# Kernel tuning notes

Hardware: AMD Instinct MI355X
Metric: run time of the kernel (lower is better)

The kernel has to match this reference:

```python
import jax, jax.numpy as jnp
import numpy as np

N_NODES = 5000
N_EDGES = 80000
HIDDEN = 128
NUM_RBF = 64
MAX_Z = 128
CUTOFF_UPPER = 5.0
LN_EPS = 1e-5


def setup_inputs() -> dict:
    key = jax.random.key(0)
    ks = jax.random.split(key, 24)
    H, R = HIDDEN, NUM_RBF
    def lin(k, out_d, in_d):
        s = 1.0 / np.sqrt(in_d)
        return jax.random.uniform(k, (out_d, in_d), jnp.float32, -s, s)
    def bias(k, out_d, in_d):
        s = 1.0 / np.sqrt(in_d)
        return jax.random.uniform(k, (out_d,), jnp.float32, -s, s)
    v = jax.random.normal(ks[3], (N_EDGES, 3), jnp.float32)
    v = v / jnp.linalg.norm(v, axis=-1, keepdims=True)
    return {
        "z": jax.random.randint(ks[0], (N_NODES,), 0, MAX_Z),
        "edge_index": jax.random.randint(ks[1], (2, N_EDGES), 0, N_NODES),
        "edge_weight": jax.random.uniform(ks[2], (N_EDGES,), jnp.float32) * CUTOFF_UPPER * 0.9,
        "edge_vec_norm": v,
        "edge_attr": jax.random.normal(ks[4], (N_EDGES, R), jnp.float32),
        "emb": jax.random.normal(ks[5], (MAX_Z, H), jnp.float32),
        "W_emb2": lin(ks[6], H, 2 * H), "b_emb2": bias(ks[7], H, 2 * H),
        "Wd1": lin(ks[8], H, R), "bd1": bias(ks[9], H, R),
        "Wd2": lin(ks[10], H, R), "bd2": bias(ks[11], H, R),
        "Wd3": lin(ks[12], H, R), "bd3": bias(ks[13], H, R),
        "Wt1": lin(ks[14], H, H), "Wt2": lin(ks[15], H, H), "Wt3": lin(ks[16], H, H),
        "Ws1": lin(ks[17], 2 * H, H), "bs1": bias(ks[18], 2 * H, H),
        "Ws2": lin(ks[19], 3 * H, 2 * H), "bs2": bias(ks[20], 3 * H, 2 * H),
        "ln_g": jnp.ones((H,), jnp.float32),
        "ln_b": jnp.zeros((H,), jnp.float32),
    }


def _skew(v):
    # v: [E,3] -> [E,3,3] skew-symmetric
    z = jnp.zeros_like(v[:, 0])
    return jnp.stack(
        [z, -v[:, 2], v[:, 1], v[:, 2], z, -v[:, 0], -v[:, 1], v[:, 0], z], axis=1
    ).reshape(-1, 3, 3)


def _sym(v):
    # symmetric traceless part of outer product (outer product already symmetric)
    outer = v[:, :, None] * v[:, None, :]
    tr = jnp.trace(outer, axis1=-2, axis2=-1) / 3.0
    return outer - tr[:, None, None] * jnp.eye(3, dtype=v.dtype)


def reference(z, edge_index, edge_weight, edge_vec_norm, edge_attr,
              emb, W_emb2, b_emb2, Wd1, bd1, Wd2, bd2, Wd3, bd3,
              Wt1, Wt2, Wt3, Ws1, bs1, Ws2, bs2, ln_g, ln_b):
    N = z.shape[0]
    H = emb.shape[1]
    src, dst = edge_index[0], edge_index[1]

    # atomic number message Zij: [E,H]
    Z = emb[z]
    Zij = jnp.concatenate([Z[src], Z[dst]], axis=-1) @ W_emb2.T + b_emb2

    # cosine cutoff (cutoff_lower = 0)
    cut = 0.5 * (jnp.cos(edge_weight * (jnp.pi / CUTOFF_UPPER)) + 1.0)
    cut = cut * (edge_weight < CUTOFF_UPPER).astype(edge_weight.dtype)
    C = cut[:, None] * Zij  # [E,H]

    f1 = (edge_attr @ Wd1.T + bd1) * C  # [E,H]
    f2 = (edge_attr @ Wd2.T + bd2) * C
    f3 = (edge_attr @ Wd3.T + bd3) * C

    eye = jnp.eye(3, dtype=C.dtype)
    Iij = f1[:, :, None, None] * eye  # [E,H,3,3]
    Aij = f2[:, :, None, None] * _skew(edge_vec_norm)[:, None, :, :]
    Sij = f3[:, :, None, None] * _sym(edge_vec_norm)[:, None, :, :]

    I = jax.ops.segment_sum(Iij, src, num_segments=N)  # [N,H,3,3]
    A = jax.ops.segment_sum(Aij, src, num_segments=N)
    S = jax.ops.segment_sum(Sij, src, num_segments=N)

    # Frobenius norm per channel, LayerNorm, scalar MLP
    tn = ((I + A + S) ** 2).sum((-2, -1))  # [N,H]
    mu = tn.mean(-1, keepdims=True)
    var = tn.var(-1, keepdims=True)
    norm = (tn - mu) / jnp.sqrt(var + LN_EPS) * ln_g + ln_b
    norm = jax.nn.silu(norm @ Ws1.T + bs1)
    norm = jax.nn.silu(norm @ Ws2.T + bs2)
    norm = norm.reshape(N, H, 3)

    I = jnp.einsum('nhij,gh->ngij', I, Wt1) * norm[:, :, 0, None, None]
    A = jnp.einsum('nhij,gh->ngij', A, Wt2) * norm[:, :, 1, None, None]
    S = jnp.einsum('nhij,gh->ngij', S, Wt3) * norm[:, :, 2, None, None]
    return I + A + S
```

## Files before the change

kernel.cpp:

```cpp
#include <hip/hip_runtime.h>
#include <hip/hip_bf16.h>

#define NN   5000
#define NP   5008
#define NE   80000
#define HID  128
#define NRBF 64
#define PI_OVER_5 0.6283185307179586f
#define LN_EPS 1e-5f

typedef unsigned short bf16_t;
typedef __attribute__((ext_vector_type(8))) short short8;
typedef __attribute__((ext_vector_type(4))) float floatx4;

__device__ __forceinline__ bf16_t to_bf16(float x){
    union { float f; unsigned int u; } v; v.f = x;
    unsigned int r = v.u + 0x7fffu + ((v.u >> 16) & 1u);
    return (bf16_t)(r >> 16);
}
__device__ __forceinline__ float from_bf16(bf16_t h){
    union { unsigned int u; float f; } v; v.u = ((unsigned int)h) << 16;
    return v.f;
}
__device__ __forceinline__ uint4 pack8(const float* s){
    float4 a = *(const float4*)s;
    float4 b = *(const float4*)(s + 4);
    uint4 o;
    o.x = to_bf16(a.x) | ((unsigned)to_bf16(a.y) << 16);
    o.y = to_bf16(a.z) | ((unsigned)to_bf16(a.w) << 16);
    o.z = to_bf16(b.x) | ((unsigned)to_bf16(b.y) << 16);
    o.w = to_bf16(b.z) | ((unsigned)to_bf16(b.w) << 16);
    return o;
}
__device__ __forceinline__ short8 cvt8(float4 a, float4 b){
    short8 r;
    r[0] = (short)to_bf16(a.x); r[1] = (short)to_bf16(a.y);
    r[2] = (short)to_bf16(a.z); r[3] = (short)to_bf16(a.w);
    r[4] = (short)to_bf16(b.x); r[5] = (short)to_bf16(b.y);
    r[6] = (short)to_bf16(b.z); r[7] = (short)to_bf16(b.w);
    return r;
}

__global__ __launch_bounds__(256) void k_prep(
    const float* __restrict__ Wd1, const float* __restrict__ Wd2, const float* __restrict__ Wd3,
    const float* __restrict__ bd1, const float* __restrict__ bd2, const float* __restrict__ bd3,
    const float* __restrict__ Wt1, const float* __restrict__ Wt2, const float* __restrict__ Wt3,
    const float* __restrict__ Ws1, const float* __restrict__ Ws2,
    const float* __restrict__ W_emb2, const float* __restrict__ emb,
    bf16_t* __restrict__ Wcat, bf16_t* __restrict__ Wtc,
    bf16_t* __restrict__ Ws1b, bf16_t* __restrict__ Ws2b, float* __restrict__ bdcat,
    float* __restrict__ embL, float* __restrict__ embR)
{
    int b = blockIdx.x, tid = threadIdx.x;
    if (b < 100){
        int t = b * 256 + tid;
        int i8 = t * 8;
        const float* src; bf16_t* dst;
        if (i8 < 24576){
            int j = i8; int tb = j >> 13; int r = j & 8191;
            src = ((tb == 0) ? Wd1 : (tb == 1) ? Wd2 : Wd3) + r; dst = Wcat + j;
        } else if (i8 < 24576 + 49152){
            int j = i8 - 24576; int tb = j >> 14; int r = j & 16383;
            src = ((tb == 0) ? Wt1 : (tb == 1) ? Wt2 : Wt3) + r; dst = Wtc + j;
        } else if (i8 < 24576 + 49152 + 32768){
            int j = i8 - 73728; src = Ws1 + j; dst = Ws1b + j;
        } else {
            int j = i8 - 106496; src = Ws2 + j; dst = Ws2b + j;
        }
        *(uint4*)dst = pack8(src);
        if (t < 384){
            int tb2 = t >> 7, ch2 = t & 127;
            const float* bsrc = (tb2 == 0) ? bd1 : ((tb2 == 1) ? bd2 : bd3);
            bdcat[t] = bsrc[ch2];
        }
    } else {
        int t = b - 100;
        int half = tid >> 7;
        int h = tid & 127;
        const float* wl = W_emb2 + (size_t)h * (2 * HID) + half * HID;
        const float* er = emb + t * HID;
        float s = 0.f;
        #pragma unroll 8
        for (int k = 0; k < HID; k++) s += wl[k] * er[k];
        (half ? embR : embL)[t * HID + h] = s;
    }
}

__global__ void k_count(const int* __restrict__ ei, int* __restrict__ counts){
    int e = blockIdx.x * 256 + threadIdx.x;
    if (e < NE) atomicAdd(&counts[ei[e]], 1);
}

__global__ __launch_bounds__(1024) void k_scan(
    const int* __restrict__ counts, int* __restrict__ offsets, int* __restrict__ cursor)
{
    __shared__ int s[1024];
    const int t = threadIdx.x;
    const int CH = 5;
    int base = t * CH;
    int loc[CH];
    int lsum = 0;
    #pragma unroll
    for (int u = 0; u < CH; u++){
        int i = base + u;
        int v = (i < NN) ? counts[i] : 0;
        loc[u] = lsum;
        lsum += v;
    }
    s[t] = lsum;
    __syncthreads();
    for (int d = 1; d < 1024; d <<= 1){
        int v = (t >= d) ? s[t - d] : 0;
        __syncthreads();
        s[t] += v;
        __syncthreads();
    }
    int excl = s[t] - lsum;
    #pragma unroll
    for (int u = 0; u < CH; u++){
        int i = base + u;
        if (i < NN){ int o = excl + loc[u]; offsets[i] = o; cursor[i] = o; }
    }
    if (t == 1023) offsets[NN] = s[1023];
}

__global__ void k_fill(const int* __restrict__ ei, const int* __restrict__ z,
                       const float* __restrict__ ew, const float* __restrict__ evn,
                       int* __restrict__ cursor, int* __restrict__ elist,
                       float2* __restrict__ meta, float* __restrict__ evn_p){
    int e = blockIdx.x * 256 + threadIdx.x;
    if (e < NE){
        int sN = ei[e], dN = ei[NE + e];
        int p = atomicAdd(&cursor[sN], 1);
        elist[p] = e;
        float w = ew[e];
        float c = (w < 5.0f) ? 0.5f * (__cosf(w * PI_OVER_5) + 1.0f) : 0.0f;
        meta[p] = make_float2(c, __int_as_float(z[sN] | (z[dN] << 8)));
        evn_p[p*3+0] = evn[e*3+0];
        evn_p[p*3+1] = evn[e*3+1];
        evn_p[p*3+2] = evn[e*3+2];
    }
}

__global__ __launch_bounds__(256) void k_edge_gather(
    const int* __restrict__ offs, const int* __restrict__ elist,
    const float2* __restrict__ meta, const float* __restrict__ evn_p,
    const float* __restrict__ attr,
    const bf16_t* __restrict__ Wcat, const float* __restrict__ bdcat,
    const float* __restrict__ embL, const float* __restrict__ embR,
    const float* __restrict__ b_emb2,
    const float* __restrict__ ln_g, const float* __restrict__ ln_b,
    bf16_t* __restrict__ accb, bf16_t* __restrict__ lnb)
{
    __shared__ __align__(16) float4 sV[64];
    __shared__ int   sZZ[64];
    __shared__ float sAcc[10][132];
    __shared__ float sRed[8];

    const int tid = threadIdx.x;
    const int wv = tid >> 6, lane = tid & 63;
    const int col = lane & 15, q = lane >> 4;
    const int n = blockIdx.x;
    const int s = offs[n], e_end = offs[n + 1];

    short8 bfr[6][2];
    float bdv[3][2], bev[2];
    #pragma unroll
    for (int cg = 0; cg < 2; cg++){
        int ch = wv * 32 + cg * 16 + col;
        bev[cg] = b_emb2[ch];
        #pragma unroll
        for (int t = 0; t < 3; t++){
            bdv[t][cg] = bdcat[t * 128 + ch];
            #pragma unroll
            for (int s2 = 0; s2 < 2; s2++)
                bfr[t * 2 + cg][s2] = *(const short8*)(Wcat + (size_t)(t * 128 + ch) * NRBF + s2 * 32 + q * 8);
        }
    }

    float pl[10][2];
    #pragma unroll
    for (int p = 0; p < 10; p++){ pl[p][0] = 0.f; pl[p][1] = 0.f; }

    for (int c0 = s; c0 < e_end; c0 += 64){
        __syncthreads();
        if (tid < 64){
            int pos = c0 + tid;
            if (pos < e_end){
                float2 m = meta[pos];
                sV[tid]  = make_float4(evn_p[pos*3+0], evn_p[pos*3+1], evn_p[pos*3+2], m.x);
                sZZ[tid] = __float_as_int(m.y);
            } else {
                sV[tid]  = make_float4(0.f, 0.f, 0.f, 0.f);
                sZZ[tid] = 0;
            }
        }
        __syncthreads();
        int nch = e_end - c0; if (nch > 64) nch = 64;
        int ntiles = (nch + 15) >> 4;
        for (int t16 = 0; t16 < ntiles; t16++){
            int pos = c0 + t16 * 16 + col;
            int cpos = (pos < e_end) ? pos : (e_end - 1);
            int e = elist[cpos];
            const float* ar = attr + (size_t)e * NRBF + q * 8;
            short8 af[2];
            #pragma unroll
            for (int s2 = 0; s2 < 2; s2++){
                float4 u0 = *(const float4*)(ar + s2 * 32);
                float4 u1 = *(const float4*)(ar + s2 * 32 + 4);
                af[s2] = cvt8(u0, u1);
            }
            floatx4 D[3][2];
            #pragma unroll
            for (int t = 0; t < 3; t++)
                #pragma unroll
                for (int cg = 0; cg < 2; cg++){
                    floatx4 d = (floatx4)(0.f);
                    d = __builtin_amdgcn_mfma_f32_16x16x32_bf16(af[0], bfr[t*2+cg][0], d, 0, 0, 0);
                    d = __builtin_amdgcn_mfma_f32_16x16x32_bf16(af[1], bfr[t*2+cg][1], d, 0, 0, 0);
                    D[t][cg] = d;
                }
            #pragma unroll
            for (int r = 0; r < 4; r++){
                int eslot = t16 * 16 + q * 4 + r;
                float4 vv = sV[eslot];
                int zp = sZZ[eslot];
                int zs = zp & 255, zd = zp >> 8;
                float vx = vv.x, vy = vv.y, vz = vv.z, cut = vv.w;
                float xx = vx*vx, yy = vy*vy, zz = vz*vz;
                float t3 = (xx + yy + zz) * (1.f/3.f);
                float gxx = xx - t3, gyy = yy - t3, gzz = zz - t3;
                float gxy = vx*vy, gxz = vx*vz, gyz = vy*vz;
                #pragma unroll
                for (int cg = 0; cg < 2; cg++){
                    int ch = wv * 32 + cg * 16 + col;
                    float L = embL[zs * HID + ch];
                    float R = embR[zd * HID + ch];
                    float Cv = cut * (L + R + bev[cg]);
                    float f1 = (D[0][cg][r] + bdv[0][cg]) * Cv;
                    float f2 = (D[1][cg][r] + bdv[1][cg]) * Cv;
                    float f3 = (D[2][cg][r] + bdv[2][cg]) * Cv;
                    pl[0][cg] += f1;
                    pl[1][cg] += f2 * vx; pl[2][cg] += f2 * vy; pl[3][cg] += f2 * vz;
                    pl[4][cg] += f3 * gxx; pl[5][cg] += f3 * gyy; pl[6][cg] += f3 * gzz;
                    pl[7][cg] += f3 * gxy; pl[8][cg] += f3 * gxz; pl[9][cg] += f3 * gyz;
                }
            }
        }
    }

    #pragma unroll
    for (int p = 0; p < 10; p++)
        #pragma unroll
        for (int cg = 0; cg < 2; cg++){
            float v = pl[p][cg];
            v += __shfl_xor(v, 16);
            v += __shfl_xor(v, 32);
            pl[p][cg] = v;
        }
    if (lane < 16){
        #pragma unroll
        for (int p = 0; p < 10; p++){
            sAcc[p][wv * 32 + 0  + lane] = pl[p][0];
            sAcc[p][wv * 32 + 16 + lane] = pl[p][1];
        }
    }
    __syncthreads();

    float av[10]; float tn = 0.f;
    const int ch = tid;
    if (tid < 128){
        #pragma unroll
        for (int p = 0; p < 10; p++) av[p] = sAcc[p][ch];
        tn = 3.f*av[0]*av[0] + 2.f*av[0]*(av[4]+av[5]+av[6])
           + av[4]*av[4] + av[5]*av[5] + av[6]*av[6]
           + 2.f*(av[7]*av[7] + av[8]*av[8] + av[9]*av[9])
           + 2.f*(av[1]*av[1] + av[2]*av[2] + av[3]*av[3]);
    }
    float s1 = tn, s2 = tn * tn;
    #pragma unroll
    for (int d = 1; d < 64; d <<= 1){
        s1 += __shfl_xor(s1, d);
        s2 += __shfl_xor(s2, d);
    }
    if (lane == 0){ sRed[wv] = s1; sRed[4 + wv] = s2; }
    __syncthreads();
    if (tid < 128){
        float mu  = (sRed[0] + sRed[1]) * (1.f / HID);
        float var = (sRed[4] + sRed[5]) * (1.f / HID) - mu * mu;
        float ln = (tn - mu) * rsqrtf(var + LN_EPS) * ln_g[ch] + ln_b[ch];
        lnb[(size_t)n * HID + ch] = to_bf16(ln);
        #pragma unroll
        for (int p = 0; p < 10; p++)
            accb[(size_t)p * NP * HID + (size_t)n * HID + ch] = to_bf16(av[p]);
    }
}

__global__ __launch_bounds__(256) void k_node(
    const bf16_t* __restrict__ lnb, const bf16_t* __restrict__ accb,
    const bf16_t* __restrict__ Ws1b, const float* __restrict__ bs1,
    const bf16_t* __restrict__ Ws2b, const float* __restrict__ bs2,
    const bf16_t* __restrict__ Wtc,
    float* __restrict__ out)
{
    __shared__ __align__(16) bf16_t h1s[16 * 280];
    __shared__ float nrms[16 * 392];

    const int tid = threadIdx.x;
    const int wv = tid >> 6, lane = tid & 63;
    const int col = lane & 15, q = lane >> 4;
    const int n0 = blockIdx.x * 16;

    {
        short8 a1[4];
        #pragma unroll
        for (int k = 0; k < 4; k++)
            a1[k] = *(const short8*)(lnb + (size_t)(n0 + col) * HID + k * 32 + q * 8);
        floatx4 c1[4];
        #pragma unroll
        for (int nt = 0; nt < 4; nt++) c1[nt] = (floatx4)(0.f);
        #pragma unroll
        for (int nt = 0; nt < 4; nt++){
            int cg = wv * 64 + nt * 16 + col;
            #pragma unroll
            for (int k = 0; k < 4; k++){
                short8 b = *(const short8*)(Ws1b + (size_t)cg * HID + k * 32 + q * 8);
                c1[nt] = __builtin_amdgcn_mfma_f32_16x16x32_bf16(a1[k], b, c1[nt], 0, 0, 0);
            }
        }
        #pragma unroll
        for (int nt = 0; nt < 4; nt++){
            int cg = wv * 64 + nt * 16 + col;
            float bias = bs1[cg];
            #pragma unroll
            for (int r = 0; r < 4; r++){
                float v = c1[nt][r] + bias;
                v = v / (1.f + __expf(-v));
                h1s[(q * 4 + r) * 280 + cg] = to_bf16(v);
            }
        }
    }
    __syncthreads();

    {
        short8 a2[8];
        #pragma unroll
        for (int k = 0; k < 8; k++)
            a2[k] = *(const short8*)&h1s[col * 280 + k * 32 + q * 8];
        floatx4 c2[6];
        #pragma unroll
        for (int nt = 0; nt < 6; nt++) c2[nt] = (floatx4)(0.f);
        #pragma unroll
        for (int nt = 0; nt < 6; nt++){
            int cg = wv * 96 + nt * 16 + col;
            #pragma unroll
            for (int k = 0; k < 8; k++){
                short8 b = *(const short8*)(Ws2b + (size_t)cg * 256 + k * 32 + q * 8);
                c2[nt] = __builtin_amdgcn_mfma_f32_16x16x32_bf16(a2[k], b, c2[nt], 0, 0, 0);
            }
        }
        #pragma unroll
        for (int nt = 0; nt < 6; nt++){
            int cg = wv * 96 + nt * 16 + col;
            float bias = bs2[cg];
            #pragma unroll
            for (int r = 0; r < 4; r++){
                float v = c2[nt][r] + bias;
                v = v / (1.f + __expf(-v));
                nrms[(q * 4 + r) * 392 + cg] = v;
            }
        }
    }
    __syncthreads();

    floatx4 cm[10][2];
    #pragma unroll
    for (int p = 0; p < 10; p++){
        #pragma unroll
        for (int nt = 0; nt < 2; nt++) cm[p][nt] = (floatx4)(0.f);
    }
    #pragma unroll
    for (int p = 0; p < 10; p++){
        const bf16_t* ap = accb + (size_t)p * NP * HID + (size_t)(n0 + col) * HID;
        short8 a3[4];
        #pragma unroll
        for (int k = 0; k < 4; k++)
            a3[k] = *(const short8*)(ap + k * 32 + q * 8);
        int tb = (p == 0) ? 0 : ((p < 4) ? 1 : 2);
        #pragma unroll
        for (int nt = 0; nt < 2; nt++){
            int g = wv * 32 + nt * 16 + col;
            const bf16_t* wp = Wtc + tb * 16384 + (size_t)g * HID;
            #pragma unroll
            for (int k = 0; k < 4; k++){
                short8 b = *(const short8*)(wp + k * 32 + q * 8);
                cm[p][nt] = __builtin_amdgcn_mfma_f32_16x16x32_bf16(a3[k], b, cm[p][nt], 0, 0, 0);
            }
        }
    }
    #pragma unroll
    for (int nt = 0; nt < 2; nt++){
        int g = wv * 32 + nt * 16 + col;
        #pragma unroll
        for (int r = 0; r < 4; r++){
            int node = q * 4 + r;
            int n = n0 + node;
            if (n < NN){
                float n0f = nrms[node * 392 + g * 3 + 0];
                float n1f = nrms[node * 392 + g * 3 + 1];
                float n2f = nrms[node * 392 + g * 3 + 2];
                float c   = cm[0][nt][r];
                float ax  = cm[1][nt][r], ay = cm[2][nt][r], az = cm[3][nt][r];
                float sxx = cm[4][nt][r], syy= cm[5][nt][r], szz= cm[6][nt][r];
                float sxy = cm[7][nt][r], sxz= cm[8][nt][r], syz= cm[9][nt][r];
                float* o = out + ((size_t)n * HID + g) * 9;
                o[0] = n0f*c + n2f*sxx;   o[1] = n2f*sxy - n1f*az;  o[2] = n2f*sxz + n1f*ay;
                o[3] = n2f*sxy + n1f*az;  o[4] = n0f*c + n2f*syy;   o[5] = n2f*syz - n1f*ax;
                o[6] = n2f*sxz - n1f*ay;  o[7] = n2f*syz + n1f*ax;  o[8] = n0f*c + n2f*szz;
            }
        }
    }
}

extern "C" void kernel_launch(void* const* d_in, const int* in_sizes, int n_in,
                              void* d_out, int out_size, void* d_ws, size_t ws_size,
                              hipStream_t stream)
{
    (void)in_sizes; (void)n_in; (void)out_size; (void)ws_size;
    const int*   z      = (const int*)  d_in[0];
    const int*   ei     = (const int*)  d_in[1];
    const float* ew     = (const float*)d_in[2];
    const float* evn    = (const float*)d_in[3];
    const float* attr   = (const float*)d_in[4];
    const float* emb    = (const float*)d_in[5];
    const float* W_emb2 = (const float*)d_in[6];
    const float* b_emb2 = (const float*)d_in[7];
    const float* Wd1 = (const float*)d_in[8];  const float* bd1 = (const float*)d_in[9];
    const float* Wd2 = (const float*)d_in[10]; const float* bd2 = (const float*)d_in[11];
    const float* Wd3 = (const float*)d_in[12]; const float* bd3 = (const float*)d_in[13];
    const float* Wt1 = (const float*)d_in[14]; const float* Wt2 = (const float*)d_in[15];
    const float* Wt3 = (const float*)d_in[16];
    const float* Ws1 = (const float*)d_in[17]; const float* bs1 = (const float*)d_in[18];
    const float* Ws2 = (const float*)d_in[19]; const float* bs2 = (const float*)d_in[20];
    const float* ln_g = (const float*)d_in[21]; const float* ln_b = (const float*)d_in[22];
    float* out = (float*)d_out;

    char* ws = (char*)d_ws;
    size_t o = 0;
    auto take = [&](size_t b)->size_t{ size_t c = o; o += (b + 255) & ~(size_t)255; return c; };
    size_t acc_o = take((size_t)10 * NP * HID * 2);
    size_t ln_of = take((size_t)NP * HID * 2);
    size_t eL_o  = take((size_t)128 * HID * 4);
    size_t eR_o  = take((size_t)128 * HID * 4);
    size_t cnt_o = take((size_t)NN * 4);
    size_t off_o = take((size_t)(NN + 1) * 4);
    size_t cur_o = take((size_t)NN * 4);
    size_t el_o  = take((size_t)NE * 4);
    size_t met_o = take((size_t)NE * 8);
    size_t evp_o = take((size_t)NE * 12);
    size_t wc_o  = take((size_t)384 * 64 * 2);
    size_t wt_o  = take((size_t)3 * 128 * 128 * 2);
    size_t w1_o  = take((size_t)256 * 128 * 2);
    size_t w2_o  = take((size_t)384 * 256 * 2);
    size_t bdc_o = take((size_t)384 * 4);

    bf16_t* accb = (bf16_t*)(ws + acc_o);
    bf16_t* lnb  = (bf16_t*)(ws + ln_of);
    float* embL = (float*)(ws + eL_o);
    float* embR = (float*)(ws + eR_o);
    int* counts = (int*)(ws + cnt_o);
    int* offs   = (int*)(ws + off_o);
    int* cursor = (int*)(ws + cur_o);
    int* elist  = (int*)(ws + el_o);
    float2* meta = (float2*)(ws + met_o);
    float* evn_p = (float*)(ws + evp_o);
    bf16_t* Wcat = (bf16_t*)(ws + wc_o);
    bf16_t* Wtc  = (bf16_t*)(ws + wt_o);
    bf16_t* Ws1b = (bf16_t*)(ws + w1_o);
    bf16_t* Ws2b = (bf16_t*)(ws + w2_o);
    float* bdcat = (float*)(ws + bdc_o);

    hipMemsetAsync(counts, 0, (size_t)NN * 4, stream);

    k_prep <<<228, 256, 0, stream>>>(Wd1, Wd2, Wd3, bd1, bd2, bd3,
                                     Wt1, Wt2, Wt3, Ws1, Ws2, W_emb2, emb,
                                     Wcat, Wtc, Ws1b, Ws2b, bdcat, embL, embR);
    k_count<<<(NE + 255) / 256, 256, 0, stream>>>(ei, counts);
    k_scan <<<1, 1024, 0, stream>>>(counts, offs, cursor);
    k_fill <<<(NE + 255) / 256, 256, 0, stream>>>(ei, z, ew, evn, cursor, elist, meta, evn_p);
    k_edge_gather<<<NN, 256, 0, stream>>>(offs, elist, meta, evn_p, attr,
                                          Wcat, bdcat, embL, embR, b_emb2,
                                          ln_g, ln_b, accb, lnb);
    k_node <<<(NN + 15) / 16, 256, 0, stream>>>(lnb, accb, Ws1b, bs1, Ws2b, bs2, Wtc, out);
}
```

Measured before the change: 242.3 us.

## Process eight nodes per edge-gather block and fold edge counting into prep

The edge-gather kernel now handles 8 consecutive destination nodes per block instead of one. Their edges are processed as one contiguous stream, and each lane accumulates partial sums per run of same-node edges, then flushes them into a per-node shared-memory accumulator with LDS atomics. This spreads the per-block weight-fragment loads and setup over more edges and removes the tail waste of nearly empty 64-edge chunks per node, at the cost of shared-memory atomics and fewer, larger blocks. The separate edge-count kernel is merged into the prep kernel as extra blocks, removing one launch.

```diff
diff --git a/kernel.cpp b/kernel.cpp
--- a/kernel.cpp
+++ b/kernel.cpp
@@ -6,6 +6,7 @@
 #define NE   80000
 #define HID  128
 #define NRBF 64
+#define NPB  8
 #define PI_OVER_5 0.6283185307179586f
 #define LN_EPS 1e-5f
 
@@ -47,6 +48,7 @@
     const float* __restrict__ Wt1, const float* __restrict__ Wt2, const float* __restrict__ Wt3,
     const float* __restrict__ Ws1, const float* __restrict__ Ws2,
     const float* __restrict__ W_emb2, const float* __restrict__ emb,
+    const int* __restrict__ ei, int* __restrict__ counts,
     bf16_t* __restrict__ Wcat, bf16_t* __restrict__ Wtc,
     bf16_t* __restrict__ Ws1b, bf16_t* __restrict__ Ws2b, float* __restrict__ bdcat,
     float* __restrict__ embL, float* __restrict__ embR)
@@ -73,7 +75,7 @@
             const float* bsrc = (tb2 == 0) ? bd1 : ((tb2 == 1) ? bd2 : bd3);
             bdcat[t] = bsrc[ch2];
         }
-    } else {
+    } else if (b < 228){
         int t = b - 100;
         int half = tid >> 7;
         int h = tid & 127;
@@ -83,12 +85,10 @@
         #pragma unroll 8
         for (int k = 0; k < HID; k++) s += wl[k] * er[k];
         (half ? embR : embL)[t * HID + h] = s;
-    }
-}
-
-__global__ void k_count(const int* __restrict__ ei, int* __restrict__ counts){
-    int e = blockIdx.x * 256 + threadIdx.x;
-    if (e < NE) atomicAdd(&counts[ei[e]], 1);
+    } else {
+        int e = (b - 228) * 256 + tid;
+        if (e < NE) atomicAdd(&counts[ei[e]], 1);
+    }
 }
 
 __global__ __launch_bounds__(1024) void k_scan(
@@ -152,16 +152,24 @@
     const float* __restrict__ ln_g, const float* __restrict__ ln_b,
     bf16_t* __restrict__ accb, bf16_t* __restrict__ lnb)
 {
+    __shared__ float sAcc[NPB][10][HID];
     __shared__ __align__(16) float4 sV[64];
     __shared__ int   sZZ[64];
-    __shared__ float sAcc[10][132];
-    __shared__ float sRed[8];
+    __shared__ int   sLid[64];
+    __shared__ int   sOffs[NPB + 1];
+    __shared__ float sR1[NPB * 2], sR2[NPB * 2];
 
     const int tid = threadIdx.x;
     const int wv = tid >> 6, lane = tid & 63;
     const int col = lane & 15, q = lane >> 4;
-    const int n = blockIdx.x;
-    const int s = offs[n], e_end = offs[n + 1];
+    const int n0 = blockIdx.x * NPB;
+
+    if (tid <= NPB) sOffs[tid] = offs[n0 + tid];
+    {
+        float* za = &sAcc[0][0][0];
+        #pragma unroll
+        for (int i = 0; i < NPB * 10 * HID / 256; i++) za[tid + i * 256] = 0.f;
+    }
 
     short8 bfr[6][2];
     float bdv[3][2], bev[2];
@@ -177,10 +185,9 @@
                 bfr[t * 2 + cg][s2] = *(const short8*)(Wcat + (size_t)(t * 128 + ch) * NRBF + s2 * 32 + q * 8);
         }
     }
-
-    float pl[10][2];
-    #pragma unroll
-    for (int p = 0; p < 10; p++){ pl[p][0] = 0.f; pl[p][1] = 0.f; }
+    __syncthreads();
+
+    const int s = sOffs[0], e_end = sOffs[NPB];
 
     for (int c0 = s; c0 < e_end; c0 += 64){
         __syncthreads();
@@ -190,9 +197,14 @@
                 float2 m = meta[pos];
                 sV[tid]  = make_float4(evn_p[pos*3+0], evn_p[pos*3+1], evn_p[pos*3+2], m.x);
                 sZZ[tid] = __float_as_int(m.y);
+                int lid = 0;
+                #pragma unroll
+                for (int j = 1; j < NPB; j++) lid += (pos >= sOffs[j]);
+                sLid[tid] = lid;
             } else {
                 sV[tid]  = make_float4(0.f, 0.f, 0.f, 0.f);
                 sZZ[tid] = 0;
+                sLid[tid] = NPB - 1;
             }
         }
         __syncthreads();
@@ -220,9 +232,27 @@
                     d = __builtin_amdgcn_mfma_f32_16x16x32_bf16(af[1], bfr[t*2+cg][1], d, 0, 0, 0);
                     D[t][cg] = d;
                 }
+            int base = t16 * 16 + q * 4;
+            float pl[10][2];
+            #pragma unroll
+            for (int p = 0; p < 10; p++){ pl[p][0] = 0.f; pl[p][1] = 0.f; }
+            int cur = sLid[base];
             #pragma unroll
             for (int r = 0; r < 4; r++){
-                int eslot = t16 * 16 + q * 4 + r;
+                int eslot = base + r;
+                int lid = sLid[eslot];
+                if (lid != cur){
+                    #pragma unroll
+                    for (int cg = 0; cg < 2; cg++){
+                        int ch = wv * 32 + cg * 16 + col;
+                        #pragma unroll
+                        for (int p = 0; p < 10; p++){
+                            atomicAdd(&sAcc[cur][p][ch], pl[p][cg]);
+                            pl[p][cg] = 0.f;
+                        }
+                    }
+                    cur = lid;
+                }
                 float4 vv = sV[eslot];
                 int zp = sZZ[eslot];
                 int zs = zp & 255, zd = zp >> 8;
@@ -246,49 +276,43 @@
                     pl[7][cg] += f3 * gxy; pl[8][cg] += f3 * gxz; pl[9][cg] += f3 * gyz;
                 }
             }
-        }
-    }
-
-    #pragma unroll
-    for (int p = 0; p < 10; p++)
-        #pragma unroll
-        for (int cg = 0; cg < 2; cg++){
-            float v = pl[p][cg];
-            v += __shfl_xor(v, 16);
-            v += __shfl_xor(v, 32);
-            pl[p][cg] = v;
-        }
-    if (lane < 16){
-        #pragma unroll
-        for (int p = 0; p < 10; p++){
-            sAcc[p][wv * 32 + 0  + lane] = pl[p][0];
-            sAcc[p][wv * 32 + 16 + lane] = pl[p][1];
+            #pragma unroll
+            for (int cg = 0; cg < 2; cg++){
+                int ch = wv * 32 + cg * 16 + col;
+                #pragma unroll
+                for (int p = 0; p < 10; p++)
+                    atomicAdd(&sAcc[cur][p][ch], pl[p][cg]);
+            }
         }
     }
     __syncthreads();
 
-    float av[10]; float tn = 0.f;
-    const int ch = tid;
-    if (tid < 128){
-        #pragma unroll
-        for (int p = 0; p < 10; p++) av[p] = sAcc[p][ch];
-        tn = 3.f*av[0]*av[0] + 2.f*av[0]*(av[4]+av[5]+av[6])
-           + av[4]*av[4] + av[5]*av[5] + av[6]*av[6]
-           + 2.f*(av[7]*av[7] + av[8]*av[8] + av[9]*av[9])
-           + 2.f*(av[1]*av[1] + av[2]*av[2] + av[3]*av[3]);
-    }
-    float s1 = tn, s2 = tn * tn;
-    #pragma unroll
-    for (int d = 1; d < 64; d <<= 1){
-        s1 += __shfl_xor(s1, d);
-        s2 += __shfl_xor(s2, d);
-    }
-    if (lane == 0){ sRed[wv] = s1; sRed[4 + wv] = s2; }
-    __syncthreads();
-    if (tid < 128){
-        float mu  = (sRed[0] + sRed[1]) * (1.f / HID);
-        float var = (sRed[4] + sRed[5]) * (1.f / HID) - mu * mu;
+    #pragma unroll
+    for (int pair = 0; pair < 4; pair++){
+        int nl = pair * 2 + (tid >> 7);
+        int ch = tid & 127;
+        float av[10];
+        #pragma unroll
+        for (int p = 0; p < 10; p++) av[p] = sAcc[nl][p][ch];
+        float tn = 3.f*av[0]*av[0] + 2.f*av[0]*(av[4]+av[5]+av[6])
+                 + av[4]*av[4] + av[5]*av[5] + av[6]*av[6]
+                 + 2.f*(av[7]*av[7] + av[8]*av[8] + av[9]*av[9])
+                 + 2.f*(av[1]*av[1] + av[2]*av[2] + av[3]*av[3]);
+        float s1 = tn, s2 = tn * tn;
+        #pragma unroll
+        for (int d = 1; d < 64; d <<= 1){
+            s1 += __shfl_xor(s1, d);
+            s2 += __shfl_xor(s2, d);
+        }
+        if (lane == 0){
+            int slot = nl * 2 + ((tid >> 6) & 1);
+            sR1[slot] = s1; sR2[slot] = s2;
+        }
+        __syncthreads();
+        float mu  = (sR1[nl*2] + sR1[nl*2+1]) * (1.f / HID);
+        float var = (sR2[nl*2] + sR2[nl*2+1]) * (1.f / HID) - mu * mu;
         float ln = (tn - mu) * rsqrtf(var + LN_EPS) * ln_g[ch] + ln_b[ch];
+        int n = n0 + nl;
         lnb[(size_t)n * HID + ch] = to_bf16(ln);
         #pragma unroll
         for (int p = 0; p < 10; p++)
@@ -482,14 +506,13 @@
 
     hipMemsetAsync(counts, 0, (size_t)NN * 4, stream);
 
-    k_prep <<<228, 256, 0, stream>>>(Wd1, Wd2, Wd3, bd1, bd2, bd3,
-                                     Wt1, Wt2, Wt3, Ws1, Ws2, W_emb2, emb,
-                                     Wcat, Wtc, Ws1b, Ws2b, bdcat, embL, embR);
-    k_count<<<(NE + 255) / 256, 256, 0, stream>>>(ei, counts);
+    k_prep <<<228 + (NE + 255) / 256, 256, 0, stream>>>(
+        Wd1, Wd2, Wd3, bd1, bd2, bd3, Wt1, Wt2, Wt3, Ws1, Ws2, W_emb2, emb,
+        ei, counts, Wcat, Wtc, Ws1b, Ws2b, bdcat, embL, embR);
     k_scan <<<1, 1024, 0, stream>>>(counts, offs, cursor);
     k_fill <<<(NE + 255) / 256, 256, 0, stream>>>(ei, z, ew, evn, cursor, elist, meta, evn_p);
-    k_edge_gather<<<NN, 256, 0, stream>>>(offs, elist, meta, evn_p, attr,
-                                          Wcat, bdcat, embL, embR, b_emb2,
-                                          ln_g, ln_b, accb, lnb);
+    k_edge_gather<<<NN / NPB, 256, 0, stream>>>(offs, elist, meta, evn_p, attr,
+                                                Wcat, bdcat, embL, embR, b_emb2,
+                                                ln_g, ln_b, accb, lnb);
     k_node <<<(NN + 15) / 16, 256, 0, stream>>>(lnb, accb, Ws1b, bs1, Ws2b, bs2, Wtc, out);
 }
```

Result: slower. 397.5 us (+64.1%).
